# Performance work log

Hardware: AMD Instinct MI355X
Metric: run time of the kernel (lower is better)

## Reference

```python
import jax, jax.numpy as jnp
import numpy as np

B, T, IN, H, OUT = 64, 2048, 64, 512, 32


def setup_inputs() -> dict:
    key = jax.random.key(0)
    ks = jax.random.split(key, 8)
    # xavier_normal with gain=0.5: std = gain * sqrt(2/(fan_in+fan_out))
    std_fz = 0.5 * np.sqrt(2.0 / ((IN + H) + 2 * H))
    std_r = 0.5 * np.sqrt(2.0 / ((IN + H) + H))
    # nn.Linear default init: uniform(-1/sqrt(fan_in), 1/sqrt(fan_in))
    lim = 1.0 / np.sqrt(H)
    return {
        "u": jax.random.normal(ks[0], (B, T, IN), dtype=jnp.float32),
        "x0": jax.random.uniform(ks[1], (B, 1, H), dtype=jnp.float32),
        "kernel_fz": std_fz * jax.random.normal(ks[2], (IN + H, 2 * H), dtype=jnp.float32),
        "bias_fz": jnp.zeros((2 * H,), dtype=jnp.float32),
        "kernel_r": std_r * jax.random.normal(ks[3], (IN + H, H), dtype=jnp.float32),
        "bias_r": jnp.zeros((H,), dtype=jnp.float32),
        "W_out": jax.random.uniform(ks[4], (OUT, H), dtype=jnp.float32, minval=-lim, maxval=lim),
        "b_out": jax.random.uniform(ks[5], (OUT,), dtype=jnp.float32, minval=-lim, maxval=lim),
    }


def reference(u, x0, kernel_fz, bias_fz, kernel_r, bias_r, W_out, b_out):
    Hd = kernel_r.shape[1]
    x_init = x0[:, 0, :]  # [B, H]

    def step(x, u_t):
        # u_t: [B, IN], x: [B, H]
        fz = jax.nn.sigmoid(jnp.concatenate([u_t, x], axis=-1) @ kernel_fz + bias_fz)
        f, z = fz[:, :Hd], fz[:, Hd:]
        r = jnp.tanh(jnp.concatenate([u_t, f * x], axis=-1) @ kernel_r + bias_r)
        xk = (1.0 - z) * x + z * r
        y = x @ W_out.T + b_out  # output computed from PREVIOUS state, as in torch step()
        return xk, y

    u_tb = jnp.swapaxes(u, 0, 1)  # [T, B, IN]
    _, ys = jax.lax.scan(step, x_init, u_tb)  # ys: [T, B, OUT]
    return jnp.swapaxes(ys, 0, 1)  # [B, T, OUT]
```

## Files before the change

### kernel.cpp

```cpp
#include <hip/hip_runtime.h>
#include <hip/hip_fp16.h>
#include <stdint.h>

#define B_    64
#define T_    2048
#define IN_   64
#define H_    512
#define H2_   1024
#define OUT_  32
#define KTOT  576

#define NBG   8
#define NCG   32
#define NTHR  256
#define BPG   8
#define KSL   18
#define RS    12

#define ABORT_IDX   0
#define CTR_OFF     1024
#define CTR_STRIDE  1024
#define NCTR        (NBG * 2)
#define BUF_BASE    (CTR_OFF + NCTR * CTR_STRIDE)
#define XSLABW      16384

__device__ __forceinline__ unsigned f2h2(float a, float b) {
  __half2 h = __floats2half2_rn(a, b);
  unsigned r; __builtin_memcpy(&r, &h, 4); return r;
}
__device__ __forceinline__ float2 h2f2(unsigned u) {
  __half2 h; __builtin_memcpy(&h, &u, 4);
  return __half22float2(h);
}

__device__ __forceinline__ void gpubh(unsigned* p, unsigned v) {
  asm volatile("global_atomic_swap %0, %1, off sc1\n\ts_waitcnt vmcnt(0)"
               :: "v"(p), "v"(v) : "memory");
}
__device__ __forceinline__ void gaddu(unsigned* p, unsigned v) {
  asm volatile("global_atomic_add %0, %1, off sc1"
               :: "v"(p), "v"(v) : "memory");
}
__device__ __forceinline__ unsigned gpollu(const unsigned* p) {
  unsigned v;
  asm volatile("global_load_dword %0, %1, off sc0 sc1\n\ts_waitcnt vmcnt(0)"
               : "=v"(v) : "v"(p) : "memory");
  return v;
}
__device__ __forceinline__ void gload2(const unsigned* p0, const unsigned* p1,
                                       uint4& a, uint4& b) {
  asm volatile(
      "global_load_dwordx4 %0, %2, off sc0 sc1\n\t"
      "global_load_dwordx4 %1, %3, off sc0 sc1\n\t"
      "s_waitcnt vmcnt(0)"
      : "=&v"(a), "=&v"(b)
      : "v"(p0), "v"(p1)
      : "memory");
}

__global__ __launch_bounds__(256) void gru_init(float* ws, const float* __restrict__ x0) {
  int i = blockIdx.x * blockDim.x + threadIdx.x;
  int stride = gridDim.x * blockDim.x;
  unsigned* w = (unsigned*)ws;
  for (int k = i; k < BUF_BASE; k += stride) w[k] = 0u;
  unsigned* xh = w + BUF_BASE;
  for (int p = i; p < NBG * H_ * 4; p += stride) {
    int bg = p >> 11, col = (p >> 2) & (H_ - 1), f2 = p & 3;
    float v0 = x0[(bg * 8 + 2 * f2) * H_ + col];
    float v1 = x0[(bg * 8 + 2 * f2 + 1) * H_ + col];
    xh[p] = f2h2(v0, v1);
  }
}

__device__ __forceinline__ bool gbar_wait(unsigned* ctr, unsigned target,
                                          unsigned* abort_w) {
  __shared__ int s_ok;
  if (threadIdx.x == 0) {
    int ok = 1;
    int polls = 0;
    while (gpollu(ctr) < target) {
      __builtin_amdgcn_s_sleep(1);
      if ((++polls & 255) == 0) {
        if (__hip_atomic_load(abort_w, __ATOMIC_RELAXED, __HIP_MEMORY_SCOPE_AGENT) != 0u ||
            polls > 2000000) {
          __hip_atomic_store(abort_w, 1u, __ATOMIC_RELAXED, __HIP_MEMORY_SCOPE_AGENT);
          ok = 0;
          break;
        }
      }
    }
    s_ok = ok;
  }
  __syncthreads();
  __atomic_signal_fence(__ATOMIC_ACQUIRE);
  return s_ok != 0;
}

__global__ __launch_bounds__(NTHR, 1) void gru_main(
    const float* __restrict__ u, const float* __restrict__ kfz,
    const float* __restrict__ bfz, const float* __restrict__ kr,
    const float* __restrict__ br, const float* __restrict__ wout,
    const float* __restrict__ bout, float* __restrict__ out, float* ws) {
  unsigned* wsu = (unsigned*)ws;
  unsigned* abort_w = wsu + ABORT_IDX;
  unsigned* xg0 = wsu + BUF_BASE;
  unsigned* xg1 = xg0 + XSLABW;
  unsigned* xfg = xg1 + XSLABW;

  const int bg  = blockIdx.x & 7;
  const int cg  = blockIdx.x >> 3;
  const int tid = threadIdx.x;
  const int w   = tid >> 6;
  const int l   = tid & 63;
  const int cq  = l & 7;
  const int g   = l >> 3;
  const int kb  = (w * 8 + g) * KSL;
  const int fc  = tid >> 3;
  const int fb  = tid & 7;
  const int yb  = tid >> 5;
  const int yq  = tid & 31;

  unsigned* ctrA = wsu + CTR_OFF + (bg * 2 + 0) * CTR_STRIDE;
  unsigned* ctrB = wsu + CTR_OFF + (bg * 2 + 1) * CTR_STRIDE;

  __shared__ float bufA[KTOT * RS];
  __shared__ float pA[4 * 32 * RS];
  __shared__ float pB[4 * 16 * RS];
  __shared__ float rbuf[16 * 8];

  float wA[KSL][4];
#pragma unroll
  for (int i = 0; i < KSL; ++i)
#pragma unroll
    for (int m = 0; m < 4; ++m) {
      int c = 4 * cq + m;
      int gcol = (c < 16) ? (16 * cg + c) : (512 + 16 * cg + (c - 16));
      wA[i][m] = kfz[(size_t)(kb + i) * H2_ + gcol];
    }
  float wB[KSL][2];
#pragma unroll
  for (int i = 0; i < KSL; ++i)
#pragma unroll
    for (int m = 0; m < 2; ++m)
      wB[i][m] = kr[(size_t)(kb + i) * H_ + (16 * cg + 2 * cq + m)];
  float wy[16];
#pragma unroll
  for (int i = 0; i < 16; ++i) wy[i] = wout[cg * H_ + (yq + 32 * i)];
  const float by = bout[cg];
  const int fzc = (fc < 16) ? (16 * cg + fc) : (512 + 16 * cg + (fc - 16));
  const float biasA = bfz[fzc];
  const float biasB = (tid < 128) ? br[16 * cg + fc] : 0.0f;

  float zreg = 0.0f, xoldz = 0.0f;

  {
    int k2 = tid & 31, b = tid >> 5;
    float2 uv = *(const float2*)&u[((size_t)(bg * 8 + b) * T_) * IN_ + 2 * k2];
    bufA[(2 * k2) * RS + b] = uv.x;
    bufA[(2 * k2 + 1) * RS + b] = uv.y;
  }

  for (int t = 0; t < T_; ++t) {
    unsigned* xcur = (t & 1) ? xg1 : xg0;
    unsigned* xnxt = (t & 1) ? xg0 : xg1;

    {
      const unsigned* s0 = xcur + ((size_t)(bg * H_) + tid) * 4;
      const unsigned* s1 = xcur + ((size_t)(bg * H_) + tid + 256) * 4;
      uint4 a, b;
      gload2(s0, s1, a, b);
      float2 c0 = h2f2(a.x), c1 = h2f2(a.y), c2 = h2f2(a.z), c3 = h2f2(a.w);
      *(float4*)&bufA[(64 + tid) * RS]     = make_float4(c0.x, c0.y, c1.x, c1.y);
      *(float4*)&bufA[(64 + tid) * RS + 4] = make_float4(c2.x, c2.y, c3.x, c3.y);
      float2 d0 = h2f2(b.x), d1 = h2f2(b.y), d2 = h2f2(b.z), d3 = h2f2(b.w);
      *(float4*)&bufA[(64 + tid + 256) * RS]     = make_float4(d0.x, d0.y, d1.x, d1.y);
      *(float4*)&bufA[(64 + tid + 256) * RS + 4] = make_float4(d2.x, d2.y, d3.x, d3.y);
    }
    __syncthreads();

    float acc[4][8] = {};
#pragma unroll
    for (int i = 0; i < KSL; ++i) {
      const float* xr = &bufA[(kb + i) * RS];
      float4 x0 = *(const float4*)xr;
      float4 x1 = *(const float4*)(xr + 4);
#pragma unroll
      for (int m = 0; m < 4; ++m) {
        float wv = wA[i][m];
        acc[m][0] += wv * x0.x; acc[m][1] += wv * x0.y;
        acc[m][2] += wv * x0.z; acc[m][3] += wv * x0.w;
        acc[m][4] += wv * x1.x; acc[m][5] += wv * x1.y;
        acc[m][6] += wv * x1.z; acc[m][7] += wv * x1.w;
      }
    }

#pragma unroll
    for (int m = 0; m < 4; ++m)
#pragma unroll
      for (int b = 0; b < 8; ++b) {
        acc[m][b] += __shfl_xor(acc[m][b], 8);
        acc[m][b] += __shfl_xor(acc[m][b], 16);
        acc[m][b] += __shfl_xor(acc[m][b], 32);
      }
    if (g == 0) {
#pragma unroll
      for (int m = 0; m < 4; ++m) {
        float* p = &pA[(w * 32 + 4 * cq + m) * RS];
        *(float4*)p = make_float4(acc[m][0], acc[m][1], acc[m][2], acc[m][3]);
        *(float4*)(p + 4) = make_float4(acc[m][4], acc[m][5], acc[m][6], acc[m][7]);
      }
    }
    __syncthreads();

    {
      float s = pA[(0 * 32 + fc) * RS + fb] + pA[(1 * 32 + fc) * RS + fb] +
                pA[(2 * 32 + fc) * RS + fb] + pA[(3 * 32 + fc) * RS + fb] + biasA;
      float sig = 1.0f / (1.0f + __expf(-s));
      if (fc < 16) {
        float xo = bufA[(64 + 16 * cg + fc) * RS + fb];
        float v = sig * xo;
        float v1 = __shfl_xor(v, 1);
        if ((tid & 1) == 0) {
          unsigned* p = xfg + ((size_t)(bg * H_) + 16 * cg + fc) * 4 + (fb >> 1);
          gpubh(p, f2h2(v, v1));
        }
      } else {
        zreg = sig;
        xoldz = bufA[(64 + 16 * cg + (fc - 16)) * RS + fb];
      }
    }

    __syncthreads();
    if (tid == 0) gaddu(ctrA, 1u);

    {
      float yp = 0.0f;
#pragma unroll
      for (int i = 0; i < 16; ++i)
        yp += wy[i] * bufA[(64 + yq + 32 * i) * RS + yb];
      yp += __shfl_xor(yp, 1);  yp += __shfl_xor(yp, 2);
      yp += __shfl_xor(yp, 4);  yp += __shfl_xor(yp, 8);
      yp += __shfl_xor(yp, 16);
      if (yq == 0)
        out[((size_t)(bg * 8 + yb) * T_ + t) * OUT_ + cg] = yp + by;
    }

    if (!gbar_wait(ctrA, (unsigned)(NCG * (t + 1)), abort_w)) return;

    {
      const unsigned* s0 = xfg + ((size_t)(bg * H_) + tid) * 4;
      const unsigned* s1 = xfg + ((size_t)(bg * H_) + tid + 256) * 4;
      uint4 a, b;
      gload2(s0, s1, a, b);
      float2 c0 = h2f2(a.x), c1 = h2f2(a.y), c2 = h2f2(a.z), c3 = h2f2(a.w);
      *(float4*)&bufA[(64 + tid) * RS]     = make_float4(c0.x, c0.y, c1.x, c1.y);
      *(float4*)&bufA[(64 + tid) * RS + 4] = make_float4(c2.x, c2.y, c3.x, c3.y);
      float2 d0 = h2f2(b.x), d1 = h2f2(b.y), d2 = h2f2(b.z), d3 = h2f2(b.w);
      *(float4*)&bufA[(64 + tid + 256) * RS]     = make_float4(d0.x, d0.y, d1.x, d1.y);
      *(float4*)&bufA[(64 + tid + 256) * RS + 4] = make_float4(d2.x, d2.y, d3.x, d3.y);
    }
    __syncthreads();

    float acc2[2][8] = {};
#pragma unroll
    for (int i = 0; i < KSL; ++i) {
      const float* xr = &bufA[(kb + i) * RS];
      float4 x0 = *(const float4*)xr;
      float4 x1 = *(const float4*)(xr + 4);
#pragma unroll
      for (int m = 0; m < 2; ++m) {
        float wv = wB[i][m];
        acc2[m][0] += wv * x0.x; acc2[m][1] += wv * x0.y;
        acc2[m][2] += wv * x0.z; acc2[m][3] += wv * x0.w;
        acc2[m][4] += wv * x1.x; acc2[m][5] += wv * x1.y;
        acc2[m][6] += wv * x1.z; acc2[m][7] += wv * x1.w;
      }
    }
#pragma unroll
    for (int m = 0; m < 2; ++m)
#pragma unroll
      for (int b = 0; b < 8; ++b) {
        acc2[m][b] += __shfl_xor(acc2[m][b], 8);
        acc2[m][b] += __shfl_xor(acc2[m][b], 16);
        acc2[m][b] += __shfl_xor(acc2[m][b], 32);
      }
    if (g == 0) {
#pragma unroll
      for (int m = 0; m < 2; ++m) {
        float* p = &pB[(w * 16 + 2 * cq + m) * RS];
        *(float4*)p = make_float4(acc2[m][0], acc2[m][1], acc2[m][2], acc2[m][3]);
        *(float4*)(p + 4) = make_float4(acc2[m][4], acc2[m][5], acc2[m][6], acc2[m][7]);
      }
    }
    __syncthreads();

    if (tid < 128) {
      float s = pB[(0 * 16 + fc) * RS + fb] + pB[(1 * 16 + fc) * RS + fb] +
                pB[(2 * 16 + fc) * RS + fb] + pB[(3 * 16 + fc) * RS + fb] + biasB;
      float e = __expf(2.0f * s);
      rbuf[fc * 8 + fb] = 1.0f - 2.0f / (1.0f + e);
    }
    __syncthreads();

    if (tid >= 128) {
      float r = rbuf[(fc - 16) * 8 + fb];
      float xn = xoldz + zreg * (r - xoldz);
      float xn1 = __shfl_xor(xn, 1);
      if ((tid & 1) == 0) {
        unsigned* p = xnxt + ((size_t)(bg * H_) + 16 * cg + (fc - 16)) * 4 + (fb >> 1);
        gpubh(p, f2h2(xn, xn1));
      }
    }

    __syncthreads();
    if (tid == 0) gaddu(ctrB, 1u);

    if (t + 1 < T_) {
      int k2 = tid & 31, b = tid >> 5;
      float2 uv = *(const float2*)&u[((size_t)(bg * 8 + b) * T_ + (t + 1)) * IN_ + 2 * k2];
      bufA[(2 * k2) * RS + b] = uv.x;
      bufA[(2 * k2 + 1) * RS + b] = uv.y;
    }

    if (!gbar_wait(ctrB, (unsigned)(NCG * (t + 1)), abort_w)) return;
  }
}

extern "C" void kernel_launch(void* const* d_in, const int* in_sizes, int n_in,
                              void* d_out, int out_size, void* d_ws, size_t ws_size,
                              hipStream_t stream) {
  const float* u    = (const float*)d_in[0];
  const float* x0   = (const float*)d_in[1];
  const float* kfz  = (const float*)d_in[2];
  const float* bfz  = (const float*)d_in[3];
  const float* kr   = (const float*)d_in[4];
  const float* br   = (const float*)d_in[5];
  const float* wout = (const float*)d_in[6];
  const float* bout = (const float*)d_in[7];
  float* out = (float*)d_out;
  float* ws  = (float*)d_ws;

  hipLaunchKernelGGL(gru_init, dim3(64), dim3(256), 0, stream, ws, x0);
  hipLaunchKernelGGL(gru_main, dim3(NBG * NCG), dim3(NTHR), 0, stream,
                     u, kfz, bfz, kr, br, wout, bout, out, ws);
}
```

Before: 13.69 ms.

## Split batch into sixteen groups of four to double block count

```diff
diff --git a/kernel.cpp b/kernel.cpp
--- a/kernel.cpp
+++ b/kernel.cpp
@@ -10,10 +10,10 @@
 #define OUT_  32
 #define KTOT  576
 
-#define NBG   8
+#define NBG   16
 #define NCG   32
 #define NTHR  256
-#define BPG   8
+#define BPG   4
 #define KSL   18
 #define RS    12
 
@@ -22,7 +22,7 @@
 #define CTR_STRIDE  1024
 #define NCTR        (NBG * 2)
 #define BUF_BASE    (CTR_OFF + NCTR * CTR_STRIDE)
-#define XSLABW      16384
+#define XSLABW      (NBG * H_ * 2)
 
 __device__ __forceinline__ unsigned f2h2(float a, float b) {
   __half2 h = __floats2half2_rn(a, b);
@@ -33,8 +33,8 @@
   return __half22float2(h);
 }
 
-__device__ __forceinline__ void gpubh(unsigned* p, unsigned v) {
-  asm volatile("global_atomic_swap %0, %1, off sc1\n\ts_waitcnt vmcnt(0)"
+__device__ __forceinline__ void gpubh_nd(unsigned* p, unsigned v) {
+  asm volatile("global_atomic_swap %0, %1, off sc1"
                :: "v"(p), "v"(v) : "memory");
 }
 __device__ __forceinline__ void gaddu(unsigned* p, unsigned v) {
@@ -47,15 +47,9 @@
                : "=v"(v) : "v"(p) : "memory");
   return v;
 }
-__device__ __forceinline__ void gload2(const unsigned* p0, const unsigned* p1,
-                                       uint4& a, uint4& b) {
-  asm volatile(
-      "global_load_dwordx4 %0, %2, off sc0 sc1\n\t"
-      "global_load_dwordx4 %1, %3, off sc0 sc1\n\t"
-      "s_waitcnt vmcnt(0)"
-      : "=&v"(a), "=&v"(b)
-      : "v"(p0), "v"(p1)
-      : "memory");
+__device__ __forceinline__ void gload1(const unsigned* p0, uint4& a) {
+  asm volatile("global_load_dwordx4 %0, %1, off sc0 sc1\n\ts_waitcnt vmcnt(0)"
+               : "=&v"(a) : "v"(p0) : "memory");
 }
 
 __global__ __launch_bounds__(256) void gru_init(float* ws, const float* __restrict__ x0) {
@@ -64,11 +58,10 @@
   unsigned* w = (unsigned*)ws;
   for (int k = i; k < BUF_BASE; k += stride) w[k] = 0u;
   unsigned* xh = w + BUF_BASE;
-  for (int p = i; p < NBG * H_ * 4; p += stride) {
-    int bg = p >> 11, col = (p >> 2) & (H_ - 1), f2 = p & 3;
-    float v0 = x0[(bg * 8 + 2 * f2) * H_ + col];
-    float v1 = x0[(bg * 8 + 2 * f2 + 1) * H_ + col];
-    xh[p] = f2h2(v0, v1);
+  for (int p = i; p < XSLABW; p += stride) {
+    int bg = p >> 10, col = (p >> 1) & (H_ - 1), pr = p & 1;
+    int b0 = bg * BPG + 2 * pr;
+    xh[p] = f2h2(x0[b0 * H_ + col], x0[(b0 + 1) * H_ + col]);
   }
 }
 
@@ -96,7 +89,7 @@
   return s_ok != 0;
 }
 
-__global__ __launch_bounds__(NTHR, 1) void gru_main(
+__global__ __launch_bounds__(NTHR, 2) void gru_main(
     const float* __restrict__ u, const float* __restrict__ kfz,
     const float* __restrict__ bfz, const float* __restrict__ kr,
     const float* __restrict__ br, const float* __restrict__ wout,
@@ -107,18 +100,17 @@
   unsigned* xg1 = xg0 + XSLABW;
   unsigned* xfg = xg1 + XSLABW;
 
-  const int bg  = blockIdx.x & 7;
-  const int cg  = blockIdx.x >> 3;
+  const int bg  = blockIdx.x >> 5;
+  const int cg  = blockIdx.x & 31;
   const int tid = threadIdx.x;
   const int w   = tid >> 6;
   const int l   = tid & 63;
   const int cq  = l & 7;
   const int g   = l >> 3;
   const int kb  = (w * 8 + g) * KSL;
-  const int fc  = tid >> 3;
-  const int fb  = tid & 7;
-  const int yb  = tid >> 5;
-  const int yq  = tid & 31;
+  const int fcA = (tid >> 2) & 31;
+  const int fb  = tid & 3;
+  const int fcB = (tid >> 2) & 15;
 
   unsigned* ctrA = wsu + CTR_OFF + (bg * 2 + 0) * CTR_STRIDE;
   unsigned* ctrB = wsu + CTR_OFF + (bg * 2 + 1) * CTR_STRIDE;
@@ -126,7 +118,7 @@
   __shared__ float bufA[KTOT * RS];
   __shared__ float pA[4 * 32 * RS];
   __shared__ float pB[4 * 16 * RS];
-  __shared__ float rbuf[16 * 8];
+  __shared__ float rbuf[16 * 4];
 
   float wA[KSL][4];
 #pragma unroll
@@ -143,21 +135,19 @@
 #pragma unroll
     for (int m = 0; m < 2; ++m)
       wB[i][m] = kr[(size_t)(kb + i) * H_ + (16 * cg + 2 * cq + m)];
-  float wy[16];
-#pragma unroll
-  for (int i = 0; i < 16; ++i) wy[i] = wout[cg * H_ + (yq + 32 * i)];
+  float wy[8];
+#pragma unroll
+  for (int i = 0; i < 8; ++i) wy[i] = wout[cg * H_ + (l + 64 * i)];
   const float by = bout[cg];
-  const int fzc = (fc < 16) ? (16 * cg + fc) : (512 + 16 * cg + (fc - 16));
+  const int fzc = (fcA < 16) ? (16 * cg + fcA) : (512 + 16 * cg + (fcA - 16));
   const float biasA = bfz[fzc];
-  const float biasB = (tid < 128) ? br[16 * cg + fc] : 0.0f;
+  const float biasB = br[16 * cg + fcB];
 
   float zreg = 0.0f, xoldz = 0.0f;
 
   {
-    int k2 = tid & 31, b = tid >> 5;
-    float2 uv = *(const float2*)&u[((size_t)(bg * 8 + b) * T_) * IN_ + 2 * k2];
-    bufA[(2 * k2) * RS + b] = uv.x;
-    bufA[(2 * k2 + 1) * RS + b] = uv.y;
+    int k = tid & 63, b = tid >> 6;
+    bufA[k * RS + b] = u[((size_t)(bg * BPG + b) * T_) * IN_ + k];
   }
 
   for (int t = 0; t < T_; ++t) {
@@ -165,161 +155,138 @@
     unsigned* xnxt = (t & 1) ? xg0 : xg1;
 
     {
-      const unsigned* s0 = xcur + ((size_t)(bg * H_) + tid) * 4;
-      const unsigned* s1 = xcur + ((size_t)(bg * H_) + tid + 256) * 4;
-      uint4 a, b;
-      gload2(s0, s1, a, b);
+      uint4 a;
+      gload1(xcur + (size_t)bg * (H_ * 2) + tid * 4, a);
       float2 c0 = h2f2(a.x), c1 = h2f2(a.y), c2 = h2f2(a.z), c3 = h2f2(a.w);
-      *(float4*)&bufA[(64 + tid) * RS]     = make_float4(c0.x, c0.y, c1.x, c1.y);
-      *(float4*)&bufA[(64 + tid) * RS + 4] = make_float4(c2.x, c2.y, c3.x, c3.y);
-      float2 d0 = h2f2(b.x), d1 = h2f2(b.y), d2 = h2f2(b.z), d3 = h2f2(b.w);
-      *(float4*)&bufA[(64 + tid + 256) * RS]     = make_float4(d0.x, d0.y, d1.x, d1.y);
-      *(float4*)&bufA[(64 + tid + 256) * RS + 4] = make_float4(d2.x, d2.y, d3.x, d3.y);
-    }
-    __syncthreads();
-
-    float acc[4][8] = {};
+      *(float4*)&bufA[(64 + 2 * tid) * RS]     = make_float4(c0.x, c0.y, c1.x, c1.y);
+      *(float4*)&bufA[(64 + 2 * tid + 1) * RS] = make_float4(c2.x, c2.y, c3.x, c3.y);
+    }
+    __syncthreads();
+
+    float acc[4][4] = {};
 #pragma unroll
     for (int i = 0; i < KSL; ++i) {
-      const float* xr = &bufA[(kb + i) * RS];
-      float4 x0 = *(const float4*)xr;
-      float4 x1 = *(const float4*)(xr + 4);
+      float4 x0 = *(const float4*)&bufA[(kb + i) * RS];
 #pragma unroll
       for (int m = 0; m < 4; ++m) {
         float wv = wA[i][m];
         acc[m][0] += wv * x0.x; acc[m][1] += wv * x0.y;
         acc[m][2] += wv * x0.z; acc[m][3] += wv * x0.w;
-        acc[m][4] += wv * x1.x; acc[m][5] += wv * x1.y;
-        acc[m][6] += wv * x1.z; acc[m][7] += wv * x1.w;
       }
     }
 
 #pragma unroll
     for (int m = 0; m < 4; ++m)
 #pragma unroll
-      for (int b = 0; b < 8; ++b) {
+      for (int b = 0; b < 4; ++b) {
         acc[m][b] += __shfl_xor(acc[m][b], 8);
         acc[m][b] += __shfl_xor(acc[m][b], 16);
         acc[m][b] += __shfl_xor(acc[m][b], 32);
       }
     if (g == 0) {
 #pragma unroll
-      for (int m = 0; m < 4; ++m) {
-        float* p = &pA[(w * 32 + 4 * cq + m) * RS];
-        *(float4*)p = make_float4(acc[m][0], acc[m][1], acc[m][2], acc[m][3]);
-        *(float4*)(p + 4) = make_float4(acc[m][4], acc[m][5], acc[m][6], acc[m][7]);
-      }
-    }
-    __syncthreads();
-
-    {
-      float s = pA[(0 * 32 + fc) * RS + fb] + pA[(1 * 32 + fc) * RS + fb] +
-                pA[(2 * 32 + fc) * RS + fb] + pA[(3 * 32 + fc) * RS + fb] + biasA;
+      for (int m = 0; m < 4; ++m)
+        *(float4*)&pA[(w * 32 + 4 * cq + m) * RS] =
+            make_float4(acc[m][0], acc[m][1], acc[m][2], acc[m][3]);
+    }
+    __syncthreads();
+
+    if (tid < 128) {
+      float s = pA[(0 * 32 + fcA) * RS + fb] + pA[(1 * 32 + fcA) * RS + fb] +
+                pA[(2 * 32 + fcA) * RS + fb] + pA[(3 * 32 + fcA) * RS + fb] + biasA;
       float sig = 1.0f / (1.0f + __expf(-s));
-      if (fc < 16) {
-        float xo = bufA[(64 + 16 * cg + fc) * RS + fb];
-        float v = sig * xo;
+      if (fcA < 16) {
+        float v = sig * bufA[(64 + 16 * cg + fcA) * RS + fb];
         float v1 = __shfl_xor(v, 1);
-        if ((tid & 1) == 0) {
-          unsigned* p = xfg + ((size_t)(bg * H_) + 16 * cg + fc) * 4 + (fb >> 1);
-          gpubh(p, f2h2(v, v1));
-        }
+        if ((tid & 1) == 0)
+          gpubh_nd(xfg + (size_t)(bg * H_ + 16 * cg + fcA) * 2 + (fb >> 1),
+                   f2h2(v, v1));
       } else {
         zreg = sig;
-        xoldz = bufA[(64 + 16 * cg + (fc - 16)) * RS + fb];
-      }
-    }
-
-    __syncthreads();
-    if (tid == 0) gaddu(ctrA, 1u);
-
+        xoldz = bufA[(64 + 16 * cg + (fcA - 16)) * RS + fb];
+      }
+    }
+
+    float yp = 0.0f;
     {
-      float yp = 0.0f;
-#pragma unroll
-      for (int i = 0; i < 16; ++i)
-        yp += wy[i] * bufA[(64 + yq + 32 * i) * RS + yb];
+#pragma unroll
+      for (int i = 0; i < 8; ++i)
+        yp += wy[i] * bufA[(64 + l + 64 * i) * RS + w];
       yp += __shfl_xor(yp, 1);  yp += __shfl_xor(yp, 2);
       yp += __shfl_xor(yp, 4);  yp += __shfl_xor(yp, 8);
-      yp += __shfl_xor(yp, 16);
-      if (yq == 0)
-        out[((size_t)(bg * 8 + yb) * T_ + t) * OUT_ + cg] = yp + by;
-    }
+      yp += __shfl_xor(yp, 16); yp += __shfl_xor(yp, 32);
+    }
+
+    asm volatile("s_waitcnt vmcnt(0)" ::: "memory");
+    __syncthreads();
+    if (tid == 0) gaddu(ctrA, 1u);
+
+    if (l == 0)
+      out[((size_t)(bg * BPG + w) * T_ + t) * OUT_ + cg] = yp + by;
 
     if (!gbar_wait(ctrA, (unsigned)(NCG * (t + 1)), abort_w)) return;
 
     {
-      const unsigned* s0 = xfg + ((size_t)(bg * H_) + tid) * 4;
-      const unsigned* s1 = xfg + ((size_t)(bg * H_) + tid + 256) * 4;
-      uint4 a, b;
-      gload2(s0, s1, a, b);
+      uint4 a;
+      gload1(xfg + (size_t)bg * (H_ * 2) + tid * 4, a);
       float2 c0 = h2f2(a.x), c1 = h2f2(a.y), c2 = h2f2(a.z), c3 = h2f2(a.w);
-      *(float4*)&bufA[(64 + tid) * RS]     = make_float4(c0.x, c0.y, c1.x, c1.y);
-      *(float4*)&bufA[(64 + tid) * RS + 4] = make_float4(c2.x, c2.y, c3.x, c3.y);
-      float2 d0 = h2f2(b.x), d1 = h2f2(b.y), d2 = h2f2(b.z), d3 = h2f2(b.w);
-      *(float4*)&bufA[(64 + tid + 256) * RS]     = make_float4(d0.x, d0.y, d1.x, d1.y);
-      *(float4*)&bufA[(64 + tid + 256) * RS + 4] = make_float4(d2.x, d2.y, d3.x, d3.y);
-    }
-    __syncthreads();
-
-    float acc2[2][8] = {};
+      *(float4*)&bufA[(64 + 2 * tid) * RS]     = make_float4(c0.x, c0.y, c1.x, c1.y);
+      *(float4*)&bufA[(64 + 2 * tid + 1) * RS] = make_float4(c2.x, c2.y, c3.x, c3.y);
+    }
+    __syncthreads();
+
+    float acc2[2][4] = {};
 #pragma unroll
     for (int i = 0; i < KSL; ++i) {
-      const float* xr = &bufA[(kb + i) * RS];
-      float4 x0 = *(const float4*)xr;
-      float4 x1 = *(const float4*)(xr + 4);
+      float4 x0 = *(const float4*)&bufA[(kb + i) * RS];
 #pragma unroll
       for (int m = 0; m < 2; ++m) {
         float wv = wB[i][m];
         acc2[m][0] += wv * x0.x; acc2[m][1] += wv * x0.y;
         acc2[m][2] += wv * x0.z; acc2[m][3] += wv * x0.w;
-        acc2[m][4] += wv * x1.x; acc2[m][5] += wv * x1.y;
-        acc2[m][6] += wv * x1.z; acc2[m][7] += wv * x1.w;
       }
     }
 #pragma unroll
     for (int m = 0; m < 2; ++m)
 #pragma unroll
-      for (int b = 0; b < 8; ++b) {
+      for (int b = 0; b < 4; ++b) {
         acc2[m][b] += __shfl_xor(acc2[m][b], 8);
         acc2[m][b] += __shfl_xor(acc2[m][b], 16);
         acc2[m][b] += __shfl_xor(acc2[m][b], 32);
       }
     if (g == 0) {
 #pragma unroll
-      for (int m = 0; m < 2; ++m) {
-        float* p = &pB[(w * 16 + 2 * cq + m) * RS];
-        *(float4*)p = make_float4(acc2[m][0], acc2[m][1], acc2[m][2], acc2[m][3]);
-        *(float4*)(p + 4) = make_float4(acc2[m][4], acc2[m][5], acc2[m][6], acc2[m][7]);
-      }
-    }
-    __syncthreads();
-
-    if (tid < 128) {
-      float s = pB[(0 * 16 + fc) * RS + fb] + pB[(1 * 16 + fc) * RS + fb] +
-                pB[(2 * 16 + fc) * RS + fb] + pB[(3 * 16 + fc) * RS + fb] + biasB;
+      for (int m = 0; m < 2; ++m)
+        *(float4*)&pB[(w * 16 + 2 * cq + m) * RS] =
+            make_float4(acc2[m][0], acc2[m][1], acc2[m][2], acc2[m][3]);
+    }
+    __syncthreads();
+
+    if (tid < 64) {
+      float s = pB[(0 * 16 + fcB) * RS + fb] + pB[(1 * 16 + fcB) * RS + fb] +
+                pB[(2 * 16 + fcB) * RS + fb] + pB[(3 * 16 + fcB) * RS + fb] + biasB;
       float e = __expf(2.0f * s);
-      rbuf[fc * 8 + fb] = 1.0f - 2.0f / (1.0f + e);
-    }
-    __syncthreads();
-
-    if (tid >= 128) {
-      float r = rbuf[(fc - 16) * 8 + fb];
+      rbuf[fcB * 4 + fb] = 1.0f - 2.0f / (1.0f + e);
+    }
+    __syncthreads();
+
+    if (tid >= 64 && tid < 128) {
+      int zr = fcA - 16;
+      float r = rbuf[zr * 4 + fb];
       float xn = xoldz + zreg * (r - xoldz);
       float xn1 = __shfl_xor(xn, 1);
-      if ((tid & 1) == 0) {
-        unsigned* p = xnxt + ((size_t)(bg * H_) + 16 * cg + (fc - 16)) * 4 + (fb >> 1);
-        gpubh(p, f2h2(xn, xn1));
-      }
-    }
-
+      if ((tid & 1) == 0)
+        gpubh_nd(xnxt + (size_t)(bg * H_ + 16 * cg + zr) * 2 + (fb >> 1),
+                 f2h2(xn, xn1));
+    }
+
+    asm volatile("s_waitcnt vmcnt(0)" ::: "memory");
     __syncthreads();
     if (tid == 0) gaddu(ctrB, 1u);
 
     if (t + 1 < T_) {
-      int k2 = tid & 31, b = tid >> 5;
-      float2 uv = *(const float2*)&u[((size_t)(bg * 8 + b) * T_ + (t + 1)) * IN_ + 2 * k2];
-      bufA[(2 * k2) * RS + b] = uv.x;
-      bufA[(2 * k2 + 1) * RS + b] = uv.y;
+      int k = tid & 63, b = tid >> 6;
+      bufA[k * RS + b] = u[((size_t)(bg * BPG + b) * T_ + (t + 1)) * IN_ + k];
     }
 
     if (!gbar_wait(ctrB, (unsigned)(NCG * (t + 1)), abort_w)) return;
```

Measured after the change: 37.65 ms. 2.75x slower.

## Interleave two batch groups per block to hide grid barrier latency

Applied to the files above, without the earlier changes.

```diff
diff --git a/kernel.cpp b/kernel.cpp
--- a/kernel.cpp
+++ b/kernel.cpp
@@ -96,6 +96,158 @@
   return s_ok != 0;
 }
 
+#define PHASE_A(BG, BUF, ZREG, XOLDZ, CTRA, CTRB)                             \
+  {                                                                           \
+    if (!gbar_wait(CTRB, (unsigned)(NCG * t), abort_w)) return;               \
+    {                                                                         \
+      const unsigned* s0 = xcur + ((size_t)((BG) * H_) + tid) * 4;            \
+      const unsigned* s1 = xcur + ((size_t)((BG) * H_) + tid + 256) * 4;      \
+      uint4 a, b;                                                             \
+      gload2(s0, s1, a, b);                                                   \
+      float2 c0 = h2f2(a.x), c1 = h2f2(a.y), c2 = h2f2(a.z), c3 = h2f2(a.w);  \
+      *(float4*)&BUF[(64 + tid) * RS]     = make_float4(c0.x, c0.y, c1.x, c1.y); \
+      *(float4*)&BUF[(64 + tid) * RS + 4] = make_float4(c2.x, c2.y, c3.x, c3.y); \
+      float2 d0 = h2f2(b.x), d1 = h2f2(b.y), d2 = h2f2(b.z), d3 = h2f2(b.w);  \
+      *(float4*)&BUF[(64 + tid + 256) * RS]     = make_float4(d0.x, d0.y, d1.x, d1.y); \
+      *(float4*)&BUF[(64 + tid + 256) * RS + 4] = make_float4(d2.x, d2.y, d3.x, d3.y); \
+    }                                                                         \
+    __syncthreads();                                                          \
+    float acc[4][8] = {};                                                     \
+    _Pragma("unroll")                                                         \
+    for (int i = 0; i < KSL; ++i) {                                           \
+      const float* xr = &BUF[(kb + i) * RS];                                  \
+      float4 x0v = *(const float4*)xr;                                        \
+      float4 x1v = *(const float4*)(xr + 4);                                  \
+      _Pragma("unroll")                                                       \
+      for (int m = 0; m < 4; ++m) {                                           \
+        float wv = wA[i][m];                                                  \
+        acc[m][0] += wv * x0v.x; acc[m][1] += wv * x0v.y;                     \
+        acc[m][2] += wv * x0v.z; acc[m][3] += wv * x0v.w;                     \
+        acc[m][4] += wv * x1v.x; acc[m][5] += wv * x1v.y;                     \
+        acc[m][6] += wv * x1v.z; acc[m][7] += wv * x1v.w;                     \
+      }                                                                       \
+    }                                                                         \
+    _Pragma("unroll")                                                         \
+    for (int m = 0; m < 4; ++m)                                               \
+      _Pragma("unroll")                                                       \
+      for (int b = 0; b < 8; ++b) {                                           \
+        acc[m][b] += __shfl_xor(acc[m][b], 8);                                \
+        acc[m][b] += __shfl_xor(acc[m][b], 16);                               \
+        acc[m][b] += __shfl_xor(acc[m][b], 32);                               \
+      }                                                                       \
+    if (g == 0) {                                                             \
+      _Pragma("unroll")                                                       \
+      for (int m = 0; m < 4; ++m) {                                           \
+        float* pp = &pA[(w * 32 + 4 * cq + m) * RS];                          \
+        *(float4*)pp = make_float4(acc[m][0], acc[m][1], acc[m][2], acc[m][3]); \
+        *(float4*)(pp + 4) = make_float4(acc[m][4], acc[m][5], acc[m][6], acc[m][7]); \
+      }                                                                       \
+    }                                                                         \
+    __syncthreads();                                                          \
+    {                                                                         \
+      float s = pA[(0 * 32 + fc) * RS + fb] + pA[(1 * 32 + fc) * RS + fb] +   \
+                pA[(2 * 32 + fc) * RS + fb] + pA[(3 * 32 + fc) * RS + fb] + biasA; \
+      float sig = 1.0f / (1.0f + __expf(-s));                                 \
+      if (fc < 16) {                                                          \
+        float xo = BUF[(64 + 16 * cg + fc) * RS + fb];                        \
+        float v = sig * xo;                                                   \
+        float v1 = __shfl_xor(v, 1);                                          \
+        if ((tid & 1) == 0)                                                   \
+          gpubh(xfg + ((size_t)((BG) * H_) + 16 * cg + fc) * 4 + (fb >> 1),   \
+                f2h2(v, v1));                                                 \
+      } else {                                                                \
+        ZREG = sig;                                                           \
+        XOLDZ = BUF[(64 + 16 * cg + (fc - 16)) * RS + fb];                    \
+      }                                                                       \
+    }                                                                         \
+    __syncthreads();                                                          \
+    if (tid == 0) gaddu(CTRA, 1u);                                            \
+    {                                                                         \
+      float yp = 0.0f;                                                        \
+      _Pragma("unroll")                                                       \
+      for (int i = 0; i < 16; ++i)                                            \
+        yp += wy[i] * BUF[(64 + yq + 32 * i) * RS + yb];                      \
+      yp += __shfl_xor(yp, 1);  yp += __shfl_xor(yp, 2);                      \
+      yp += __shfl_xor(yp, 4);  yp += __shfl_xor(yp, 8);                      \
+      yp += __shfl_xor(yp, 16);                                               \
+      if (yq == 0)                                                            \
+        out[((size_t)((BG) * 8 + yb) * T_ + t) * OUT_ + cg] = yp + by;        \
+    }                                                                         \
+  }
+
+#define PHASE_B(BG, BUF, ZREG, XOLDZ, CTRA, CTRB)                             \
+  {                                                                           \
+    if (!gbar_wait(CTRA, (unsigned)(NCG * (t + 1)), abort_w)) return;         \
+    {                                                                         \
+      const unsigned* s0 = xfg + ((size_t)((BG) * H_) + tid) * 4;             \
+      const unsigned* s1 = xfg + ((size_t)((BG) * H_) + tid + 256) * 4;       \
+      uint4 a, b;                                                             \
+      gload2(s0, s1, a, b);                                                   \
+      float2 c0 = h2f2(a.x), c1 = h2f2(a.y), c2 = h2f2(a.z), c3 = h2f2(a.w);  \
+      *(float4*)&BUF[(64 + tid) * RS]     = make_float4(c0.x, c0.y, c1.x, c1.y); \
+      *(float4*)&BUF[(64 + tid) * RS + 4] = make_float4(c2.x, c2.y, c3.x, c3.y); \
+      float2 d0 = h2f2(b.x), d1 = h2f2(b.y), d2 = h2f2(b.z), d3 = h2f2(b.w);  \
+      *(float4*)&BUF[(64 + tid + 256) * RS]     = make_float4(d0.x, d0.y, d1.x, d1.y); \
+      *(float4*)&BUF[(64 + tid + 256) * RS + 4] = make_float4(d2.x, d2.y, d3.x, d3.y); \
+    }                                                                         \
+    __syncthreads();                                                          \
+    float acc2[2][8] = {};                                                    \
+    _Pragma("unroll")                                                         \
+    for (int i = 0; i < KSL; ++i) {                                           \
+      const float* xr = &BUF[(kb + i) * RS];                                  \
+      float4 x0v = *(const float4*)xr;                                        \
+      float4 x1v = *(const float4*)(xr + 4);                                  \
+      _Pragma("unroll")                                                       \
+      for (int m = 0; m < 2; ++m) {                                           \
+        float wv = wB[i][m];                                                  \
+        acc2[m][0] += wv * x0v.x; acc2[m][1] += wv * x0v.y;                   \
+        acc2[m][2] += wv * x0v.z; acc2[m][3] += wv * x0v.w;                   \
+        acc2[m][4] += wv * x1v.x; acc2[m][5] += wv * x1v.y;                   \
+        acc2[m][6] += wv * x1v.z; acc2[m][7] += wv * x1v.w;                   \
+      }                                                                       \
+    }                                                                         \
+    _Pragma("unroll")                                                         \
+    for (int m = 0; m < 2; ++m)                                               \
+      _Pragma("unroll")                                                       \
+      for (int b = 0; b < 8; ++b) {                                           \
+        acc2[m][b] += __shfl_xor(acc2[m][b], 8);                              \
+        acc2[m][b] += __shfl_xor(acc2[m][b], 16);                             \
+        acc2[m][b] += __shfl_xor(acc2[m][b], 32);                             \
+      }                                                                       \
+    if (g == 0) {                                                             \
+      _Pragma("unroll")                                                       \
+      for (int m = 0; m < 2; ++m) {                                           \
+        float* pp = &pB[(w * 16 + 2 * cq + m) * RS];                          \
+        *(float4*)pp = make_float4(acc2[m][0], acc2[m][1], acc2[m][2], acc2[m][3]); \
+        *(float4*)(pp + 4) = make_float4(acc2[m][4], acc2[m][5], acc2[m][6], acc2[m][7]); \
+      }                                                                       \
+    }                                                                         \
+    __syncthreads();                                                          \
+    if (tid < 128) {                                                          \
+      float s = pB[(0 * 16 + fc) * RS + fb] + pB[(1 * 16 + fc) * RS + fb] +   \
+                pB[(2 * 16 + fc) * RS + fb] + pB[(3 * 16 + fc) * RS + fb] + biasB; \
+      float e = __expf(2.0f * s);                                             \
+      rbuf[fc * 8 + fb] = 1.0f - 2.0f / (1.0f + e);                           \
+    }                                                                         \
+    __syncthreads();                                                          \
+    if (tid >= 128) {                                                         \
+      float r = rbuf[(fc - 16) * 8 + fb];                                     \
+      float xn = XOLDZ + ZREG * (r - XOLDZ);                                  \
+      float xn1 = __shfl_xor(xn, 1);                                          \
+      if ((tid & 1) == 0)                                                     \
+        gpubh(xnxt + ((size_t)((BG) * H_) + 16 * cg + (fc - 16)) * 4 + (fb >> 1), \
+              f2h2(xn, xn1));                                                 \
+    }                                                                         \
+    __syncthreads();                                                          \
+    if (tid == 0) gaddu(CTRB, 1u);                                            \
+    if (t + 1 < T_) {                                                         \
+      int k2 = tid & 31, b = tid >> 5;                                        \
+      float2 uv = *(const float2*)&u[((size_t)((BG) * 8 + b) * T_ + (t + 1)) * IN_ + 2 * k2]; \
+      BUF[(2 * k2) * RS + b] = uv.x;                                          \
+      BUF[(2 * k2 + 1) * RS + b] = uv.y;                                      \
+    }                                                                         \
+  }
+
 __global__ __launch_bounds__(NTHR, 1) void gru_main(
     const float* __restrict__ u, const float* __restrict__ kfz,
     const float* __restrict__ bfz, const float* __restrict__ kr,
@@ -107,8 +259,9 @@
   unsigned* xg1 = xg0 + XSLABW;
   unsigned* xfg = xg1 + XSLABW;
 
-  const int bg  = blockIdx.x & 7;
-  const int cg  = blockIdx.x >> 3;
+  const int bgp = blockIdx.x & 3;
+  const int cg  = blockIdx.x >> 2;
+  const int bg0 = 2 * bgp, bg1 = 2 * bgp + 1;
   const int tid = threadIdx.x;
   const int w   = tid >> 6;
   const int l   = tid & 63;
@@ -120,10 +273,13 @@
   const int yb  = tid >> 5;
   const int yq  = tid & 31;
 
-  unsigned* ctrA = wsu + CTR_OFF + (bg * 2 + 0) * CTR_STRIDE;
-  unsigned* ctrB = wsu + CTR_OFF + (bg * 2 + 1) * CTR_STRIDE;
-
-  __shared__ float bufA[KTOT * RS];
+  unsigned* ctrA0 = wsu + CTR_OFF + (bg0 * 2 + 0) * CTR_STRIDE;
+  unsigned* ctrB0 = wsu + CTR_OFF + (bg0 * 2 + 1) * CTR_STRIDE;
+  unsigned* ctrA1 = wsu + CTR_OFF + (bg1 * 2 + 0) * CTR_STRIDE;
+  unsigned* ctrB1 = wsu + CTR_OFF + (bg1 * 2 + 1) * CTR_STRIDE;
+
+  __shared__ float buf0[KTOT * RS];
+  __shared__ float buf1[KTOT * RS];
   __shared__ float pA[4 * 32 * RS];
   __shared__ float pB[4 * 16 * RS];
   __shared__ float rbuf[16 * 8];
@@ -151,178 +307,27 @@
   const float biasA = bfz[fzc];
   const float biasB = (tid < 128) ? br[16 * cg + fc] : 0.0f;
 
-  float zreg = 0.0f, xoldz = 0.0f;
+  float zreg0 = 0.0f, xoldz0 = 0.0f;
+  float zreg1 = 0.0f, xoldz1 = 0.0f;
 
   {
     int k2 = tid & 31, b = tid >> 5;
-    float2 uv = *(const float2*)&u[((size_t)(bg * 8 + b) * T_) * IN_ + 2 * k2];
-    bufA[(2 * k2) * RS + b] = uv.x;
-    bufA[(2 * k2 + 1) * RS + b] = uv.y;
+    float2 uv = *(const float2*)&u[((size_t)(bg0 * 8 + b) * T_) * IN_ + 2 * k2];
+    buf0[(2 * k2) * RS + b] = uv.x;
+    buf0[(2 * k2 + 1) * RS + b] = uv.y;
+    float2 uw = *(const float2*)&u[((size_t)(bg1 * 8 + b) * T_) * IN_ + 2 * k2];
+    buf1[(2 * k2) * RS + b] = uw.x;
+    buf1[(2 * k2 + 1) * RS + b] = uw.y;
   }
 
   for (int t = 0; t < T_; ++t) {
     unsigned* xcur = (t & 1) ? xg1 : xg0;
     unsigned* xnxt = (t & 1) ? xg0 : xg1;
 
-    {
-      const unsigned* s0 = xcur + ((size_t)(bg * H_) + tid) * 4;
-      const unsigned* s1 = xcur + ((size_t)(bg * H_) + tid + 256) * 4;
-      uint4 a, b;
-      gload2(s0, s1, a, b);
-      float2 c0 = h2f2(a.x), c1 = h2f2(a.y), c2 = h2f2(a.z), c3 = h2f2(a.w);
-      *(float4*)&bufA[(64 + tid) * RS]     = make_float4(c0.x, c0.y, c1.x, c1.y);
-      *(float4*)&bufA[(64 + tid) * RS + 4] = make_float4(c2.x, c2.y, c3.x, c3.y);
-      float2 d0 = h2f2(b.x), d1 = h2f2(b.y), d2 = h2f2(b.z), d3 = h2f2(b.w);
-      *(float4*)&bufA[(64 + tid + 256) * RS]     = make_float4(d0.x, d0.y, d1.x, d1.y);
-      *(float4*)&bufA[(64 + tid + 256) * RS + 4] = make_float4(d2.x, d2.y, d3.x, d3.y);
-    }
-    __syncthreads();
-
-    float acc[4][8] = {};
-#pragma unroll
-    for (int i = 0; i < KSL; ++i) {
-      const float* xr = &bufA[(kb + i) * RS];
-      float4 x0 = *(const float4*)xr;
-      float4 x1 = *(const float4*)(xr + 4);
-#pragma unroll
-      for (int m = 0; m < 4; ++m) {
-        float wv = wA[i][m];
-        acc[m][0] += wv * x0.x; acc[m][1] += wv * x0.y;
-        acc[m][2] += wv * x0.z; acc[m][3] += wv * x0.w;
-        acc[m][4] += wv * x1.x; acc[m][5] += wv * x1.y;
-        acc[m][6] += wv * x1.z; acc[m][7] += wv * x1.w;
-      }
-    }
-
-#pragma unroll
-    for (int m = 0; m < 4; ++m)
-#pragma unroll
-      for (int b = 0; b < 8; ++b) {
-        acc[m][b] += __shfl_xor(acc[m][b], 8);
-        acc[m][b] += __shfl_xor(acc[m][b], 16);
-        acc[m][b] += __shfl_xor(acc[m][b], 32);
-      }
-    if (g == 0) {
-#pragma unroll
-      for (int m = 0; m < 4; ++m) {
-        float* p = &pA[(w * 32 + 4 * cq + m) * RS];
-        *(float4*)p = make_float4(acc[m][0], acc[m][1], acc[m][2], acc[m][3]);
-        *(float4*)(p + 4) = make_float4(acc[m][4], acc[m][5], acc[m][6], acc[m][7]);
-      }
-    }
-    __syncthreads();
-
-    {
-      float s = pA[(0 * 32 + fc) * RS + fb] + pA[(1 * 32 + fc) * RS + fb] +
-                pA[(2 * 32 + fc) * RS + fb] + pA[(3 * 32 + fc) * RS + fb] + biasA;
-      float sig = 1.0f / (1.0f + __expf(-s));
-      if (fc < 16) {
-        float xo = bufA[(64 + 16 * cg + fc) * RS + fb];
-        float v = sig * xo;
-        float v1 = __shfl_xor(v, 1);
-        if ((tid & 1) == 0) {
-          unsigned* p = xfg + ((size_t)(bg * H_) + 16 * cg + fc) * 4 + (fb >> 1);
-          gpubh(p, f2h2(v, v1));
-        }
-      } else {
-        zreg = sig;
-        xoldz = bufA[(64 + 16 * cg + (fc - 16)) * RS + fb];
-      }
-    }
-
-    __syncthreads();
-    if (tid == 0) gaddu(ctrA, 1u);
-
-    {
-      float yp = 0.0f;
-#pragma unroll
-      for (int i = 0; i < 16; ++i)
-        yp += wy[i] * bufA[(64 + yq + 32 * i) * RS + yb];
-      yp += __shfl_xor(yp, 1);  yp += __shfl_xor(yp, 2);
-      yp += __shfl_xor(yp, 4);  yp += __shfl_xor(yp, 8);
-      yp += __shfl_xor(yp, 16);
-      if (yq == 0)
-        out[((size_t)(bg * 8 + yb) * T_ + t) * OUT_ + cg] = yp + by;
-    }
-
-    if (!gbar_wait(ctrA, (unsigned)(NCG * (t + 1)), abort_w)) return;
-
-    {
-      const unsigned* s0 = xfg + ((size_t)(bg * H_) + tid) * 4;
-      const unsigned* s1 = xfg + ((size_t)(bg * H_) + tid + 256) * 4;
-      uint4 a, b;
-      gload2(s0, s1, a, b);
-      float2 c0 = h2f2(a.x), c1 = h2f2(a.y), c2 = h2f2(a.z), c3 = h2f2(a.w);
-      *(float4*)&bufA[(64 + tid) * RS]     = make_float4(c0.x, c0.y, c1.x, c1.y);
-      *(float4*)&bufA[(64 + tid) * RS + 4] = make_float4(c2.x, c2.y, c3.x, c3.y);
-      float2 d0 = h2f2(b.x), d1 = h2f2(b.y), d2 = h2f2(b.z), d3 = h2f2(b.w);
-      *(float4*)&bufA[(64 + tid + 256) * RS]     = make_float4(d0.x, d0.y, d1.x, d1.y);
-      *(float4*)&bufA[(64 + tid + 256) * RS + 4] = make_float4(d2.x, d2.y, d3.x, d3.y);
-    }
-    __syncthreads();
-
-    float acc2[2][8] = {};
-#pragma unroll
-    for (int i = 0; i < KSL; ++i) {
-      const float* xr = &bufA[(kb + i) * RS];
-      float4 x0 = *(const float4*)xr;
-      float4 x1 = *(const float4*)(xr + 4);
-#pragma unroll
-      for (int m = 0; m < 2; ++m) {
-        float wv = wB[i][m];
-        acc2[m][0] += wv * x0.x; acc2[m][1] += wv * x0.y;
-        acc2[m][2] += wv * x0.z; acc2[m][3] += wv * x0.w;
-        acc2[m][4] += wv * x1.x; acc2[m][5] += wv * x1.y;
-        acc2[m][6] += wv * x1.z; acc2[m][7] += wv * x1.w;
-      }
-    }
-#pragma unroll
-    for (int m = 0; m < 2; ++m)
-#pragma unroll
-      for (int b = 0; b < 8; ++b) {
-        acc2[m][b] += __shfl_xor(acc2[m][b], 8);
-        acc2[m][b] += __shfl_xor(acc2[m][b], 16);
-        acc2[m][b] += __shfl_xor(acc2[m][b], 32);
-      }
-    if (g == 0) {
-#pragma unroll
-      for (int m = 0; m < 2; ++m) {
-        float* p = &pB[(w * 16 + 2 * cq + m) * RS];
-        *(float4*)p = make_float4(acc2[m][0], acc2[m][1], acc2[m][2], acc2[m][3]);
-        *(float4*)(p + 4) = make_float4(acc2[m][4], acc2[m][5], acc2[m][6], acc2[m][7]);
-      }
-    }
-    __syncthreads();
-
-    if (tid < 128) {
-      float s = pB[(0 * 16 + fc) * RS + fb] + pB[(1 * 16 + fc) * RS + fb] +
-                pB[(2 * 16 + fc) * RS + fb] + pB[(3 * 16 + fc) * RS + fb] + biasB;
-      float e = __expf(2.0f * s);
-      rbuf[fc * 8 + fb] = 1.0f - 2.0f / (1.0f + e);
-    }
-    __syncthreads();
-
-    if (tid >= 128) {
-      float r = rbuf[(fc - 16) * 8 + fb];
-      float xn = xoldz + zreg * (r - xoldz);
-      float xn1 = __shfl_xor(xn, 1);
-      if ((tid & 1) == 0) {
-        unsigned* p = xnxt + ((size_t)(bg * H_) + 16 * cg + (fc - 16)) * 4 + (fb >> 1);
-        gpubh(p, f2h2(xn, xn1));
-      }
-    }
-
-    __syncthreads();
-    if (tid == 0) gaddu(ctrB, 1u);
-
-    if (t + 1 < T_) {
-      int k2 = tid & 31, b = tid >> 5;
-      float2 uv = *(const float2*)&u[((size_t)(bg * 8 + b) * T_ + (t + 1)) * IN_ + 2 * k2];
-      bufA[(2 * k2) * RS + b] = uv.x;
-      bufA[(2 * k2 + 1) * RS + b] = uv.y;
-    }
-
-    if (!gbar_wait(ctrB, (unsigned)(NCG * (t + 1)), abort_w)) return;
+    PHASE_A(bg0, buf0, zreg0, xoldz0, ctrA0, ctrB0)
+    PHASE_A(bg1, buf1, zreg1, xoldz1, ctrA1, ctrB1)
+    PHASE_B(bg0, buf0, zreg0, xoldz0, ctrA0, ctrB0)
+    PHASE_B(bg1, buf1, zreg1, xoldz1, ctrA1, ctrB1)
   }
 }
 
@@ -341,6 +346,6 @@
   float* ws  = (float*)d_ws;
 
   hipLaunchKernelGGL(gru_init, dim3(64), dim3(256), 0, stream, ws, x0);
-  hipLaunchKernelGGL(gru_main, dim3(NBG * NCG), dim3(NTHR), 0, stream,
+  hipLaunchKernelGGL(gru_main, dim3(4 * NCG), dim3(NTHR), 0, stream,
                      u, kfz, bfz, kr, br, wout, bout, out, ws);
 }
```

New measurement: 27.94 ms. 2.04x slower.

## Replace atomic-add group barrier counters with per-block flag slots polled in parallel

Applied to the files above, without the earlier changes.

```diff
diff --git a/kernel.cpp b/kernel.cpp
--- a/kernel.cpp
+++ b/kernel.cpp
@@ -18,10 +18,10 @@
 #define RS    12
 
 #define ABORT_IDX   0
-#define CTR_OFF     1024
-#define CTR_STRIDE  1024
-#define NCTR        (NBG * 2)
-#define BUF_BASE    (CTR_OFF + NCTR * CTR_STRIDE)
+#define FLAG_STRIDE 256
+#define FLAGS_OFF   1024
+#define FLAG_WORDS  (NBG * 2 * NCG * FLAG_STRIDE)
+#define BUF_BASE    (FLAGS_OFF + FLAG_WORDS)
 #define XSLABW      16384
 
 __device__ __forceinline__ unsigned f2h2(float a, float b) {
@@ -37,8 +37,8 @@
   asm volatile("global_atomic_swap %0, %1, off sc1\n\ts_waitcnt vmcnt(0)"
                :: "v"(p), "v"(v) : "memory");
 }
-__device__ __forceinline__ void gaddu(unsigned* p, unsigned v) {
-  asm volatile("global_atomic_add %0, %1, off sc1"
+__device__ __forceinline__ void gpubu(unsigned* p, unsigned v) {
+  asm volatile("global_atomic_swap %0, %1, off sc1"
                :: "v"(p), "v"(v) : "memory");
 }
 __device__ __forceinline__ unsigned gpollu(const unsigned* p) {
@@ -72,24 +72,28 @@
   }
 }
 
-__device__ __forceinline__ bool gbar_wait(unsigned* ctr, unsigned target,
+__device__ __forceinline__ bool gbar_wait(unsigned* base, unsigned target,
                                           unsigned* abort_w) {
   __shared__ int s_ok;
-  if (threadIdx.x == 0) {
-    int ok = 1;
+  const int tid = threadIdx.x;
+  int ok = 1;
+  if (tid < NCG) {
+    const unsigned* f = base + tid * FLAG_STRIDE;
     int polls = 0;
-    while (gpollu(ctr) < target) {
-      __builtin_amdgcn_s_sleep(1);
+    while (gpollu(f) < target) {
       if ((++polls & 255) == 0) {
         if (__hip_atomic_load(abort_w, __ATOMIC_RELAXED, __HIP_MEMORY_SCOPE_AGENT) != 0u ||
-            polls > 2000000) {
+            polls > 4000000) {
           __hip_atomic_store(abort_w, 1u, __ATOMIC_RELAXED, __HIP_MEMORY_SCOPE_AGENT);
           ok = 0;
           break;
         }
       }
     }
-    s_ok = ok;
+  }
+  if (tid < 64) {
+    unsigned long long bad = __ballot(ok == 0);
+    if (tid == 0) s_ok = (bad == 0ull) ? 1 : 0;
   }
   __syncthreads();
   __atomic_signal_fence(__ATOMIC_ACQUIRE);
@@ -103,6 +107,7 @@
     const float* __restrict__ bout, float* __restrict__ out, float* ws) {
   unsigned* wsu = (unsigned*)ws;
   unsigned* abort_w = wsu + ABORT_IDX;
+  unsigned* flags = wsu + FLAGS_OFF;
   unsigned* xg0 = wsu + BUF_BASE;
   unsigned* xg1 = xg0 + XSLABW;
   unsigned* xfg = xg1 + XSLABW;
@@ -120,8 +125,10 @@
   const int yb  = tid >> 5;
   const int yq  = tid & 31;
 
-  unsigned* ctrA = wsu + CTR_OFF + (bg * 2 + 0) * CTR_STRIDE;
-  unsigned* ctrB = wsu + CTR_OFF + (bg * 2 + 1) * CTR_STRIDE;
+  unsigned* slotA = flags + ((bg * 2 + 0) * NCG + cg) * FLAG_STRIDE;
+  unsigned* slotB = flags + ((bg * 2 + 1) * NCG + cg) * FLAG_STRIDE;
+  unsigned* baseA = flags + (bg * 2 + 0) * NCG * FLAG_STRIDE;
+  unsigned* baseB = flags + (bg * 2 + 1) * NCG * FLAG_STRIDE;
 
   __shared__ float bufA[KTOT * RS];
   __shared__ float pA[4 * 32 * RS];
@@ -231,7 +238,7 @@
     }
 
     __syncthreads();
-    if (tid == 0) gaddu(ctrA, 1u);
+    if (tid == 0) gpubu(slotA, (unsigned)(t + 1));
 
     {
       float yp = 0.0f;
@@ -245,7 +252,7 @@
         out[((size_t)(bg * 8 + yb) * T_ + t) * OUT_ + cg] = yp + by;
     }
 
-    if (!gbar_wait(ctrA, (unsigned)(NCG * (t + 1)), abort_w)) return;
+    if (!gbar_wait(baseA, (unsigned)(t + 1), abort_w)) return;
 
     {
       const unsigned* s0 = xfg + ((size_t)(bg * H_) + tid) * 4;
@@ -313,7 +320,7 @@
     }
 
     __syncthreads();
-    if (tid == 0) gaddu(ctrB, 1u);
+    if (tid == 0) gpubu(slotB, (unsigned)(t + 1));
 
     if (t + 1 < T_) {
       int k2 = tid & 31, b = tid >> 5;
@@ -322,7 +329,7 @@
       bufA[(2 * k2 + 1) * RS + b] = uv.y;
     }
 
-    if (!gbar_wait(ctrB, (unsigned)(NCG * (t + 1)), abort_w)) return;
+    if (!gbar_wait(baseB, (unsigned)(t + 1), abort_w)) return;
   }
 }
 
```

Measured after the change: 14.03 ms. 1.02x slower.
